# Kernel optimization log

Hardware: AMD Instinct MI355X
Metric: run time of the kernel (lower is better)

The kernel has to match this reference:

```python
import jax, jax.numpy as jnp
import numpy as np

# config constants (from init_kwargs)
DT = 1.0
TAU_J = 10.0
TAU_M = 20.0
KAPPA_J = 0.25
A_GEN = 1.0
A_DISC = 1.0
THRESH = 0.4
X_DECAY = 20.0  # trace decay constant: x += -x/20 + spikes

B = 8192
LS = [1024, 512, 512, 256]


def setup_inputs() -> dict:
    key = jax.random.key(0)
    ks = jax.random.split(key, 24)
    inp = {}
    inp['x_input'] = (jax.random.uniform(ks[0], (B, LS[0])) < 0.2).astype(jnp.float32)
    inp['y_target'] = (jax.random.uniform(ks[1], (B, LS[3])) < 0.2).astype(jnp.float32)
    # hidden-layer states (layers 1 and 2); layer 0 / last are clamped
    inp['j1'] = jax.random.normal(ks[2], (B, LS[1])) * 0.1
    inp['v1'] = jax.random.normal(ks[3], (B, LS[1])) * 0.1
    inp['s1'] = (jax.random.uniform(ks[4], (B, LS[1])) < 0.2).astype(jnp.float32)
    inp['x1'] = jax.random.uniform(ks[5], (B, LS[1])) * 2.0
    inp['j2'] = jax.random.normal(ks[6], (B, LS[2])) * 0.1
    inp['v2'] = jax.random.normal(ks[7], (B, LS[2])) * 0.1
    inp['s2'] = (jax.random.uniform(ks[8], (B, LS[2])) < 0.2).astype(jnp.float32)
    inp['x2'] = jax.random.uniform(ks[9], (B, LS[2])) * 2.0
    # weights (torch.rand * 0.01)
    inp['W0'] = jax.random.uniform(ks[10], (LS[0], LS[1])) * 0.01
    inp['W1'] = jax.random.uniform(ks[11], (LS[1], LS[2])) * 0.01
    inp['W2'] = jax.random.uniform(ks[12], (LS[2], LS[3])) * 0.01
    inp['V0'] = jax.random.uniform(ks[13], (LS[1], LS[0])) * 0.01
    inp['V1'] = jax.random.uniform(ks[14], (LS[2], LS[1])) * 0.01
    inp['V2'] = jax.random.uniform(ks[15], (LS[3], LS[2])) * 0.01
    inp['Eg0'] = jax.random.uniform(ks[16], (LS[1], LS[0])) * 0.01
    inp['Eg1'] = jax.random.uniform(ks[17], (LS[2], LS[1])) * 0.01
    inp['Eg2'] = jax.random.uniform(ks[18], (LS[3], LS[2])) * 0.01
    inp['Ed0'] = jax.random.uniform(ks[19], (LS[0], LS[1])) * 0.01
    inp['Ed1'] = jax.random.uniform(ks[20], (LS[1], LS[2])) * 0.01
    inp['Ed2'] = jax.random.uniform(ks[21], (LS[2], LS[3])) * 0.01
    return inp


def _lif_update(j, v, x, total_input):
    # Eq 19-24: leaky current integrator -> leaky membrane -> threshold -> reset -> trace
    j = j + (DT / TAU_J) * (-KAPPA_J * j + total_input)
    v = v + (DT / TAU_M) * (-v + j)  # uses updated j, as in the torch code
    spikes = (v > THRESH).astype(v.dtype)
    v = v * (1.0 - spikes)  # hard reset
    x = x + (-x / X_DECAY + spikes)  # spike trace
    return j, v, spikes, x


def reference(x_input, y_target, j1, v1, s1, x1, j2, v2, s2, x2,
              W0, W1, W2, V0, V1, V2, Eg0, Eg1, Eg2, Ed0, Ed1, Ed2):
    # --- phase 1: error neurons (all layers, using current spikes) ---
    # layer 0 clamped: x0 = x_input, s0 = x_input; layer 3 clamped: x3 = s3 = y_target
    e_gen0 = A_GEN * (x_input - s1 @ W0.T)       # [B, 1024]
    e_gen1 = A_GEN * (x1 - s2 @ W1.T)            # [B, 512]
    e_gen2 = A_GEN * (x2 - y_target @ W2.T)      # [B, 512]
    e_disc1 = A_DISC * (x1 - x_input @ V0.T)     # [B, 512]
    e_disc2 = A_DISC * (x2 - s1 @ V1.T)          # [B, 512]
    e_disc3 = A_DISC * (y_target - s2 @ V2.T)    # [B, 256]

    # --- phase 2: value-neuron updates (hidden layers 1 and 2 only) ---
    total1 = -(e_gen1 + e_disc1) + e_gen0 @ Eg0.T + e_disc2 @ Ed1.T
    total2 = -(e_gen2 + e_disc2) + e_gen1 @ Eg1.T + e_disc3 @ Ed2.T

    j1n, v1n, s1n, x1n = _lif_update(j1, v1, x1, total1)
    j2n, v2n, s2n, x2n = _lif_update(j2, v2, x2, total2)

    return jnp.concatenate([j1n, v1n, x1n, s1n, j2n, v2n, x2n, s2n], axis=-1)  # [B, 4096]
```

## Files before the change

### kernel.cpp

```cpp
#include <hip/hip_runtime.h>
#include <stdint.h>
#include <stddef.h>

typedef unsigned short u16;
typedef __attribute__((ext_vector_type(8))) short short8;
typedef __attribute__((ext_vector_type(4))) float f32x4;

#define DEVI __device__ __forceinline__

DEVI u16 f2bf(float f) {
  union { float f; unsigned u; } c; c.f = f;
  unsigned r = c.u + 0x7fff + ((c.u >> 16) & 1);
  return (u16)(r >> 16);
}

DEVI short8 pack8(f32x4 a, f32x4 b) {
  short8 v;
#pragma unroll
  for (int i = 0; i < 4; i++) { v[i] = (short)f2bf(a[i]); v[i + 4] = (short)f2bf(b[i]); }
  return v;
}

typedef __attribute__((address_space(1))) const void global_cvoid;
typedef __attribute__((address_space(3))) void lds_void;


DEVI void mfma_phase(const u16* As, const u16* Bs, f32x4 acc[4][4])
{
  const int lane = threadIdx.x & 63;
  const int w    = threadIdx.x >> 6;
  const int l16  = lane & 15, lq = lane >> 4;
  const int wm   = (w >> 1) * 64, wn = (w & 1) * 64;
#pragma unroll
  for (int kc = 0; kc < 2; kc++) {
    short8 afr[4], bfr[4];
#pragma unroll
    for (int rt = 0; rt < 4; rt++) {
      int m  = wm + rt * 16 + l16;
      int gr = (kc * 4 + lq) ^ (m & 7);
      afr[rt] = *(const short8*)(As + m * 64 + gr * 8);
    }
#pragma unroll
    for (int ct = 0; ct < 4; ct++) {
      int n  = wn + ct * 16 + l16;
      int gr = (kc * 4 + lq) ^ (n & 7);
      bfr[ct] = *(const short8*)(Bs + n * 64 + gr * 8);
    }
#pragma unroll
    for (int rt = 0; rt < 4; rt++)
#pragma unroll
      for (int ct = 0; ct < 4; ct++)
        acc[rt][ct] = __builtin_amdgcn_mfma_f32_16x16x32_bf16(afr[rt], bfr[ct], acc[rt][ct], 0, 0, 0);
  }
}

DEVI void mfma_phase32(const u16* As, const u16* Bs, f32x4 acc[2][2])
{
  const int lane = threadIdx.x & 63;
  const int w    = threadIdx.x >> 6;
  const int l16  = lane & 15, lq = lane >> 4;
  const int wm   = (w >> 1) * 32, wn = (w & 1) * 32;
#pragma unroll
  for (int kc = 0; kc < 2; kc++) {
    short8 afr[2], bfr[2];
#pragma unroll
    for (int rt = 0; rt < 2; rt++) {
      int m  = wm + rt * 16 + l16;
      int gr = (kc * 4 + lq) ^ (m & 7);
      afr[rt] = *(const short8*)(As + m * 64 + gr * 8);
    }
#pragma unroll
    for (int ct = 0; ct < 2; ct++) {
      int n  = wn + ct * 16 + l16;
      int gr = (kc * 4 + lq) ^ (n & 7);
      bfr[ct] = *(const short8*)(Bs + n * 64 + gr * 8);
    }
#pragma unroll
    for (int rt = 0; rt < 2; rt++)
#pragma unroll
      for (int ct = 0; ct < 2; ct++)
        acc[rt][ct] = __builtin_amdgcn_mfma_f32_16x16x32_bf16(afr[rt], bfr[ct], acc[rt][ct], 0, 0, 0);
  }
}

DEVI void mfma_phase64(const u16* As, const u16* Bs, f32x4 acc[2][4])
{
  const int lane = threadIdx.x & 63;
  const int w    = threadIdx.x >> 6;
  const int l16  = lane & 15, lq = lane >> 4;
  const int wm   = (w >> 1) * 32, wn = (w & 1) * 64;
#pragma unroll
  for (int kc = 0; kc < 2; kc++) {
    short8 afr[2], bfr[4];
#pragma unroll
    for (int rt = 0; rt < 2; rt++) {
      int m  = wm + rt * 16 + l16;
      int gr = (kc * 4 + lq) ^ (m & 7);
      afr[rt] = *(const short8*)(As + m * 64 + gr * 8);
    }
#pragma unroll
    for (int ct = 0; ct < 4; ct++) {
      int n  = wn + ct * 16 + l16;
      int gr = (kc * 4 + lq) ^ (n & 7);
      bfr[ct] = *(const short8*)(Bs + n * 64 + gr * 8);
    }
#pragma unroll
    for (int rt = 0; rt < 2; rt++)
#pragma unroll
      for (int ct = 0; ct < 4; ct++)
        acc[rt][ct] = __builtin_amdgcn_mfma_f32_16x16x32_bf16(afr[rt], bfr[ct], acc[rt][ct], 0, 0, 0);
  }
}

DEVI void zero_acc(f32x4 acc[4][4]) {
  f32x4 z = {0.f, 0.f, 0.f, 0.f};
#pragma unroll
  for (int a = 0; a < 4; a++)
#pragma unroll
    for (int b = 0; b < 4; b++) acc[a][b] = z;
}

DEVI void zero_acc22(f32x4 acc[2][2]) {
  f32x4 z = {0.f, 0.f, 0.f, 0.f};
#pragma unroll
  for (int a = 0; a < 2; a++)
#pragma unroll
    for (int b = 0; b < 2; b++) acc[a][b] = z;
}

DEVI void zero_acc24(f32x4 acc[2][4]) {
  f32x4 z = {0.f, 0.f, 0.f, 0.f};
#pragma unroll
  for (int a = 0; a < 2; a++)
#pragma unroll
    for (int b = 0; b < 4; b++) acc[a][b] = z;
}

struct Params {
  const float *x_input, *y_target, *j1, *v1, *s1, *x1, *j2, *v2, *s2, *x2;
  const float *W0, *W1, *W2, *V0, *V1, *V2, *Eg0, *Eg1, *Ed1, *Ed2;
};


template <int RR>
DEVI void stage_async(const u16* gbase, int ldr, int k0, u16* lds)
{
  const int t = threadIdx.x;
  const int lane = t & 63, w = t >> 6;
#pragma unroll
  for (int tt = 0; tt < RR; tt++) {
    int rowbase = w * (RR * 8) + tt * 8;
    int row = rowbase + (lane >> 3);
    int gsw = (lane & 7) ^ (row & 7);
    __builtin_amdgcn_global_load_lds(
        (global_cvoid*)(gbase + (size_t)row * ldr + k0 + gsw * 8),
        (lds_void*)(lds + rowbase * 64), 16, 0, 0);
  }
}

DEVI void gemm_term64(const u16* A, const u16* B, int K,
                      u16* As, u16* Bs, f32x4 acc[2][2])
{
  for (int k0 = 0; k0 < K; k0 += 64) {
    stage_async<2>(A, K, k0, As);
    stage_async<2>(B, K, k0, Bs);
    __syncthreads();
    mfma_phase32(As, Bs, acc);
    __syncthreads();
  }
}

DEVI void gemm_term_pp(const u16* A, const u16* B, int K,
                       u16* As0, u16* As1, u16* Bs0, u16* Bs1, f32x4 acc[2][4])
{
  const int nk = K >> 6;
  stage_async<2>(A, K, 0, As0);
  stage_async<4>(B, K, 0, Bs0);
  __syncthreads();
  for (int t = 0; t < nk; t++) {
    if (t + 1 < nk) {
      if (t & 1) { stage_async<2>(A, K, (t + 1) * 64, As0); stage_async<4>(B, K, (t + 1) * 64, Bs0); }
      else       { stage_async<2>(A, K, (t + 1) * 64, As1); stage_async<4>(B, K, (t + 1) * 64, Bs1); }
    }
    if (t & 1) mfma_phase64(As1, Bs1, acc);
    else       mfma_phase64(As0, Bs0, acc);
    __syncthreads();
  }
}

struct PJob { const float *s0, *s1; u16* dst; int start; };
struct TJob { const float* in; u16* out; int J, tbase; };
struct PrepArgs { PJob jb[14]; TJob tj[4]; };

__global__ __launch_bounds__(256) void k_prep(PrepArgs A)
{
  __shared__ u16 T[32][33];
  int b = blockIdx.x;
  int t = threadIdx.x;
  if (b < 14464) {
    int ji = 0;
#pragma unroll
    for (int i = 1; i < 14; i++)
      if (b >= A.jb[i].start) ji = i;
    PJob pj = A.jb[ji];
    size_t e0 = ((size_t)(b - pj.start) * 256 + t) * 8;
    const float* s0 = pj.s0 + e0;
    f32x4 a  = *(const f32x4*)s0;
    f32x4 b4 = *(const f32x4*)(s0 + 4);
    if (pj.s1) {
      const float* s1 = pj.s1 + e0;
      a  = a  + *(const f32x4*)s1;
      b4 = b4 + *(const f32x4*)(s1 + 4);
    }
    *(short8*)(pj.dst + e0) = pack8(a, b4);
    return;
  }
  int b2 = b - 14464;
  int ji = 0;
#pragma unroll
  for (int i = 1; i < 4; i++)
    if (b2 >= A.tj[i].tbase) ji = i;
  TJob jb = A.tj[ji];
  int local = b2 - jb.tbase;
  int tm = local >> 4;
  int tk = local & 15;
  int tx = t & 31, ty = t >> 5;
#pragma unroll
  for (int i = 0; i < 4; i++) {
    int r = ty + i * 8;
    T[r][tx] = f2bf(jb.in[(size_t)(tm * 32 + r) * 512 + tk * 32 + tx]);
  }
  __syncthreads();
#pragma unroll
  for (int i = 0; i < 4; i++) {
    int r = ty + i * 8;
    jb.out[(size_t)(tk * 32 + r) * jb.J + tm * 32 + tx] = T[tx][r];
  }
}

struct BW2Args {
  const u16 *Eg0b, *W0tb, *Ed1b, *V1tb, *Eg1b, *W1tb, *Ed2b, *V2tb;
  u16 *Bw1b, *Bw2b;
};

__global__ __launch_bounds__(256) void k_bw2(BW2Args A)
{
  __shared__ u16 As[64 * 64];
  __shared__ u16 Bs[64 * 64];
  int b   = blockIdx.x;
  int mat = b >> 6, loc = b & 63;
  int bmw = loc >> 3, bnw = loc & 7;

  f32x4 acc[2][2];
  zero_acc22(acc);
  u16* dst;
  if (mat == 0) {
    gemm_term64(A.Eg0b + (size_t)bmw * 64 * 1024, A.W0tb + (size_t)bnw * 64 * 1024, 1024, As, Bs, acc);
    gemm_term64(A.Ed1b + (size_t)bmw * 64 * 512,  A.V1tb + (size_t)bnw * 64 * 512,   512, As, Bs, acc);
    dst = A.Bw1b;
  } else {
    gemm_term64(A.Eg1b + (size_t)bmw * 64 * 512,  A.W1tb + (size_t)bnw * 64 * 512,   512, As, Bs, acc);
    gemm_term64(A.Ed2b + (size_t)bmw * 64 * 256,  A.V2tb + (size_t)bnw * 64 * 256,   256, As, Bs, acc);
    dst = A.Bw2b;
  }
  const int lane = threadIdx.x & 63;
  const int w    = threadIdx.x >> 6;
  const int l16  = lane & 15, lq = lane >> 4;
  const int wm   = (w >> 1) * 32, wn = (w & 1) * 32;
#pragma unroll
  for (int rt = 0; rt < 2; rt++)
#pragma unroll
    for (int ct = 0; ct < 2; ct++)
#pragma unroll
      for (int i = 0; i < 4; i++) {
        int rl = wm + rt * 16 + lq * 4 + i;
        int cl = wn + ct * 16 + l16;
        dst[(size_t)(bmw * 64 + rl) * 512 + bnw * 64 + cl] = f2bf(-acc[rt][ct][i]);
      }
}

struct MJobF {
  const u16* A[4]; const u16* B[4]; int K[4];
  const float *jin, *vin, *xin;
  int obase;
};
struct MArgsF { MJobF j[2]; };

__global__ __launch_bounds__(256, 3) void k_main_fast(MArgsF P, float* __restrict__ out)
{
  __shared__ u16 As0[64 * 64];
  __shared__ u16 As1[64 * 64];
  __shared__ u16 Bs0[128 * 64];
  __shared__ u16 Bs1[128 * 64];
  int bid   = blockIdx.x;
  int job   = bid >> 9;
  int local = bid & 511;
  int bm = local & 127, bn = local >> 7;
  MJobF jb = P.j[job];

  switch (((bid >> 8) ^ bid) & 3) {
    case 1: __builtin_amdgcn_s_sleep(8); break;
    case 2: __builtin_amdgcn_s_sleep(8); __builtin_amdgcn_s_sleep(8); break;
    case 3: __builtin_amdgcn_s_sleep(8); __builtin_amdgcn_s_sleep(8);
            __builtin_amdgcn_s_sleep(8); break;
    default: break;
  }

  f32x4 acc[2][4];
  zero_acc24(acc);
#pragma unroll
  for (int p = 0; p < 4; p++)
    gemm_term_pp(jb.A[p] + (size_t)bm * 64 * jb.K[p],
                 jb.B[p] + (size_t)bn * 128 * jb.K[p], jb.K[p],
                 As0, As1, Bs0, Bs1, acc);

  const int lane = threadIdx.x & 63;
  const int w    = threadIdx.x >> 6;
  const int l16  = lane & 15, lq = lane >> 4;
  const int wm   = (w >> 1) * 32, wn = (w & 1) * 64;

#pragma unroll
  for (int rt = 0; rt < 2; rt++)
#pragma unroll
    for (int ct = 0; ct < 4; ct++)
#pragma unroll
      for (int i = 0; i < 4; i++) {
        int row    = bm * 64 + wm + rt * 16 + lq * 4 + i;
        int col    = bn * 128 + wn + ct * 16 + l16;
        size_t idx = (size_t)row * 512 + col;
        float xf = jb.xin[idx];
        float total = acc[rt][ct][i] - 2.0f * xf;
        float jf = jb.jin[idx];
        float vf = jb.vin[idx];
        jf = jf + 0.1f * (-0.25f * jf + total);
        vf = vf + 0.05f * (-vf + jf);
        float sf = (vf > 0.4f) ? 1.0f : 0.0f;
        vf = vf * (1.0f - sf);
        xf = xf + (-xf / 20.0f + sf);
        size_t ob = (size_t)row * 4096 + jb.obase + col;
        out[ob]        = jf;
        out[ob + 512]  = vf;
        out[ob + 1024] = xf;
        out[ob + 1536] = sf;
      }
}


DEVI void stage_A_fb(const float* A, int ldr, int k0, u16* dst)
{
  const int t = threadIdx.x;
  const int g = t & 7, rb = t >> 3;
#pragma unroll
  for (int p = 0; p < 4; p++) {
    int row = p * 32 + rb;
    const float* src = A + (size_t)row * ldr + k0 + g * 8;
    f32x4 a = *(const f32x4*)src;
    f32x4 b = *(const f32x4*)(src + 4);
    *(short8*)(dst + row * 64 + (g ^ (row & 7)) * 8) = pack8(a, b);
  }
}

DEVI void nn_term_fb(const float* A, const float* B, int K, u16* As, u16* Bs, f32x4 acc[4][4])
{
  const int t  = threadIdx.x;
  const int ks = t >> 4, ng = t & 15;
  for (int k0 = 0; k0 < K; k0 += 64) {
    stage_A_fb(A, K, k0, As);
#pragma unroll
    for (int i = 0; i < 4; i++) {
      int kloc = i * 16 + ks;
      const float* src = B + (size_t)(k0 + kloc) * 512 + ng * 8;
      f32x4 a = *(const f32x4*)src;
      f32x4 b = *(const f32x4*)(src + 4);
#pragma unroll
      for (int e = 0; e < 8; e++) {
        int nloc = ng * 8 + e;
        float val = (e < 4) ? a[e] : b[e - 4];
        Bs[nloc * 64 + ((kloc >> 3) ^ (nloc & 7)) * 8 + (kloc & 7)] = f2bf(val);
      }
    }
    __syncthreads();
    mfma_phase(As, Bs, acc);
    __syncthreads();
  }
}

template <int MODE>
DEVI void gemm_term_fb(const float* A, const float* B0, const float* B1, int K,
                       u16* As, u16* Bs, f32x4 acc[4][4])
{
  const int t = threadIdx.x;
  const int g = t & 7, rb = t >> 3;
  for (int k0 = 0; k0 < K; k0 += 64) {
    stage_A_fb(A, K, k0, As);
#pragma unroll
    for (int p = 0; p < 4; p++) {
      int row = p * 32 + rb;
      const float* src;
      if (MODE == 2) src = B0 + (size_t)row * 4096 + (k0 >> 7) * 512 + (k0 & 127) + g * 8;
      else           src = B0 + (size_t)row * K + k0 + g * 8;
      f32x4 a = *(const f32x4*)src;
      f32x4 b = *(const f32x4*)(src + 4);
      if (MODE == 1) {
        const float* s2 = B1 + (size_t)row * K + k0 + g * 8;
        a = a + *(const f32x4*)s2;
        b = b + *(const f32x4*)(s2 + 4);
      }
      *(short8*)(Bs + row * 64 + (g ^ (row & 7)) * 8) = pack8(a, b);
    }
    __syncthreads();
    mfma_phase(As, Bs, acc);
    __syncthreads();
  }
}

__global__ __launch_bounds__(256) void k_bw_fb(Params P, float* __restrict__ out)
{
  __shared__ u16 As[128 * 64];
  __shared__ u16 Bs[128 * 64];
  int b   = blockIdx.x;
  int mat = b >> 4, loc = b & 15;
  int bmw = loc >> 2, bnw = loc & 3;

  f32x4 acc[4][4];
  zero_acc(acc);
  int obase;
  if (mat == 0) {
    nn_term_fb(P.Eg0 + (size_t)bmw * 128 * 1024, P.W0 + bnw * 128, 1024, As, Bs, acc);
    nn_term_fb(P.Ed1 + (size_t)bmw * 128 * 512,  P.V1 + bnw * 128,  512, As, Bs, acc);
    obase = 0;
  } else {
    nn_term_fb(P.Eg1 + (size_t)bmw * 128 * 512,  P.W1 + bnw * 128,  512, As, Bs, acc);
    nn_term_fb(P.Ed2 + (size_t)bmw * 128 * 256,  P.V2 + bnw * 128,  256, As, Bs, acc);
    obase = 2048;
  }
  const int lane = threadIdx.x & 63;
  const int w    = threadIdx.x >> 6;
  const int l16  = lane & 15, lq = lane >> 4;
  const int wm   = (w >> 1) * 64, wn = (w & 1) * 64;
#pragma unroll
  for (int rt = 0; rt < 4; rt++)
#pragma unroll
    for (int ct = 0; ct < 4; ct++)
#pragma unroll
      for (int i = 0; i < 4; i++) {
        int rl = wm + rt * 16 + lq * 4 + i;
        int cl = wn + ct * 16 + l16;
        out[(size_t)rl * 4096 + obase + bmw * 128 + bnw * 512 + cl] = -acc[rt][ct][i];
      }
}

__global__ __launch_bounds__(256) void k_main_fb(Params P, float* __restrict__ out, int fix)
{
  __shared__ u16 As[128 * 64];
  __shared__ u16 Bs[128 * 64];
  int job, bm, bn;
  if (fix) {
    job = blockIdx.x >> 2; bn = blockIdx.x & 3; bm = 0;
  } else {
    job = blockIdx.x >> 8;
    int local = blockIdx.x & 255;
    bm = local & 63; bn = local >> 6;
    if (bm == 0) return;
  }

  f32x4 acc[4][4];
  zero_acc(acc);
  const float *jin, *vin, *xin;
  int obase;
  size_t am = (size_t)bm * 128;

  if (job == 0) {
    gemm_term_fb<0>(P.s2      + am * 512,  P.W1  + (size_t)bn * 128 * 512,  nullptr, 512,  As, Bs, acc);
    gemm_term_fb<1>(P.x_input + am * 1024, P.V0  + (size_t)bn * 128 * 1024,
                    P.Eg0 + (size_t)bn * 128 * 1024, 1024, As, Bs, acc);
    gemm_term_fb<0>(P.x2      + am * 512,  P.Ed1 + (size_t)bn * 128 * 512,  nullptr, 512,  As, Bs, acc);
    gemm_term_fb<2>(P.s1      + am * 512,  out + 0 + bn * 128,              nullptr, 512,  As, Bs, acc);
    jin = P.j1; vin = P.v1; xin = P.x1; obase = 0;
  } else {
    gemm_term_fb<1>(P.y_target + am * 256, P.W2  + (size_t)bn * 128 * 256,
                    P.Ed2 + (size_t)bn * 128 * 256, 256, As, Bs, acc);
    gemm_term_fb<0>(P.s1      + am * 512,  P.V1  + (size_t)bn * 128 * 512,  nullptr, 512,  As, Bs, acc);
    gemm_term_fb<0>(P.x1      + am * 512,  P.Eg1 + (size_t)bn * 128 * 512,  nullptr, 512,  As, Bs, acc);
    gemm_term_fb<2>(P.s2      + am * 512,  out + 2048 + bn * 128,           nullptr, 512,  As, Bs, acc);
    jin = P.j2; vin = P.v2; xin = P.x2; obase = 2048;
  }

  const int lane = threadIdx.x & 63;
  const int w    = threadIdx.x >> 6;
  const int l16  = lane & 15, lq = lane >> 4;
  const int wm   = (w >> 1) * 64, wn = (w & 1) * 64;

#pragma unroll
  for (int rt = 0; rt < 4; rt++)
#pragma unroll
    for (int ct = 0; ct < 4; ct++)
#pragma unroll
      for (int i = 0; i < 4; i++) {
        int row    = bm * 128 + wm + rt * 16 + lq * 4 + i;
        int col    = bn * 128 + wn + ct * 16 + l16;
        size_t idx = (size_t)row * 512 + col;
        float xf = xin[idx];
        float total = acc[rt][ct][i] - 2.0f * xf;
        float jf = jin[idx];
        float vf = vin[idx];
        jf = jf + 0.1f * (-0.25f * jf + total);
        vf = vf + 0.05f * (-vf + jf);
        float sf = (vf > 0.4f) ? 1.0f : 0.0f;
        vf = vf * (1.0f - sf);
        xf = xf + (-xf / 20.0f + sf);
        size_t ob = (size_t)row * 4096 + obase + col;
        out[ob]        = jf;
        out[ob + 512]  = vf;
        out[ob + 1024] = xf;
        out[ob + 1536] = sf;
      }
}

extern "C" void kernel_launch(void* const* d_in, const int* in_sizes, int n_in,
                              void* d_out, int out_size, void* d_ws, size_t ws_size,
                              hipStream_t stream)
{
  Params P;
  P.x_input  = (const float*)d_in[0];
  P.y_target = (const float*)d_in[1];
  P.j1 = (const float*)d_in[2];
  P.v1 = (const float*)d_in[3];
  P.s1 = (const float*)d_in[4];
  P.x1 = (const float*)d_in[5];
  P.j2 = (const float*)d_in[6];
  P.v2 = (const float*)d_in[7];
  P.s2 = (const float*)d_in[8];
  P.x2 = (const float*)d_in[9];
  P.W0 = (const float*)d_in[10];
  P.W1 = (const float*)d_in[11];
  P.W2 = (const float*)d_in[12];
  P.V0 = (const float*)d_in[13];
  P.V1 = (const float*)d_in[14];
  P.V2 = (const float*)d_in[15];
  P.Eg0 = (const float*)d_in[16];
  P.Eg1 = (const float*)d_in[17];
  P.Ed1 = (const float*)d_in[20];
  P.Ed2 = (const float*)d_in[21];
  (void)in_sizes; (void)n_in; (void)out_size;

  float* out = (float*)d_out;

  if (ws_size >= 62652416) {
    char* ws = (char*)d_ws;
    u16* xin_b = (u16*)(ws + 0);
    u16* y_b   = (u16*)(ws + 16777216);
    u16* s1_b  = (u16*)(ws + 20971520);
    u16* x1_b  = (u16*)(ws + 29360128);
    u16* s2_b  = (u16*)(ws + 37748736);
    u16* x2_b  = (u16*)(ws + 46137344);
    u16* W1_b  = (u16*)(ws + 54525952);
    u16* P1_b  = (u16*)(ws + 55050240);
    u16* Ed1_b = (u16*)(ws + 56098816);
    u16* V1_b  = (u16*)(ws + 56623104);
    u16* Eg1_b = (u16*)(ws + 57147392);
    u16* P2_b  = (u16*)(ws + 57671680);
    u16* Bw1_b = (u16*)(ws + 57933824);
    u16* Bw2_b = (u16*)(ws + 58458112);
    u16* W0t_b = (u16*)(ws + 58982400);
    u16* V1t_b = (u16*)(ws + 60030976);
    u16* W1t_b = (u16*)(ws + 60555264);
    u16* V2t_b = (u16*)(ws + 61079552);
    u16* Eg0_b = (u16*)(ws + 61341696);
    u16* Ed2_b = (u16*)(ws + 62390272);

    PrepArgs pa;
    pa.jb[0]  = { P.x_input,  nullptr, xin_b,     0 };
    pa.jb[1]  = { P.y_target, nullptr, y_b,    4096 };
    pa.jb[2]  = { P.s1,       nullptr, s1_b,   5120 };
    pa.jb[3]  = { P.x1,       nullptr, x1_b,   7168 };
    pa.jb[4]  = { P.s2,       nullptr, s2_b,   9216 };
    pa.jb[5]  = { P.x2,       nullptr, x2_b,  11264 };
    pa.jb[6]  = { P.W1,       nullptr, W1_b,  13312 };
    pa.jb[7]  = { P.V0,       P.Eg0,   P1_b,  13440 };
    pa.jb[8]  = { P.Ed1,      nullptr, Ed1_b, 13696 };
    pa.jb[9]  = { P.V1,       nullptr, V1_b,  13824 };
    pa.jb[10] = { P.Eg1,      nullptr, Eg1_b, 13952 };
    pa.jb[11] = { P.W2,       P.Ed2,   P2_b,  14080 };
    pa.jb[12] = { P.Eg0,      nullptr, Eg0_b, 14144 };
    pa.jb[13] = { P.Ed2,      nullptr, Ed2_b, 14400 };
    pa.tj[0]  = { P.W0, W0t_b, 1024,    0 };
    pa.tj[1]  = { P.V1, V1t_b,  512,  512 };
    pa.tj[2]  = { P.W1, W1t_b,  512,  768 };
    pa.tj[3]  = { P.V2, V2t_b,  256, 1024 };
    k_prep<<<dim3(15616), dim3(256), 0, stream>>>(pa);

    BW2Args ba;
    ba.Eg0b = Eg0_b; ba.W0tb = W0t_b; ba.Ed1b = Ed1_b; ba.V1tb = V1t_b;
    ba.Eg1b = Eg1_b; ba.W1tb = W1t_b; ba.Ed2b = Ed2_b; ba.V2tb = V2t_b;
    ba.Bw1b = Bw1_b; ba.Bw2b = Bw2_b;
    k_bw2<<<dim3(128), dim3(256), 0, stream>>>(ba);

    MArgsF ma;
    ma.j[0].A[0] = s2_b;  ma.j[0].B[0] = W1_b;  ma.j[0].K[0] = 512;
    ma.j[0].A[1] = xin_b; ma.j[0].B[1] = P1_b;  ma.j[0].K[1] = 1024;
    ma.j[0].A[2] = x2_b;  ma.j[0].B[2] = Ed1_b; ma.j[0].K[2] = 512;
    ma.j[0].A[3] = s1_b;  ma.j[0].B[3] = Bw1_b; ma.j[0].K[3] = 512;
    ma.j[0].jin = P.j1; ma.j[0].vin = P.v1; ma.j[0].xin = P.x1; ma.j[0].obase = 0;
    ma.j[1].A[0] = y_b;   ma.j[1].B[0] = P2_b;  ma.j[1].K[0] = 256;
    ma.j[1].A[1] = s1_b;  ma.j[1].B[1] = V1_b;  ma.j[1].K[1] = 512;
    ma.j[1].A[2] = x1_b;  ma.j[1].B[2] = Eg1_b; ma.j[1].K[2] = 512;
    ma.j[1].A[3] = s2_b;  ma.j[1].B[3] = Bw2_b; ma.j[1].K[3] = 512;
    ma.j[1].jin = P.j2; ma.j[1].vin = P.v2; ma.j[1].xin = P.x2; ma.j[1].obase = 2048;
    k_main_fast<<<dim3(1024), dim3(256), 0, stream>>>(ma, out);
  } else {
    k_bw_fb<<<dim3(32), dim3(256), 0, stream>>>(P, out);
    k_main_fb<<<dim3(512), dim3(256), 0, stream>>>(P, out, 0);
    k_main_fb<<<dim3(8), dim3(256), 0, stream>>>(P, out, 1);
  }
}
```

Baseline: 419.0 us.

## Overlap weight-product GEMM with activation conversion; single-buffer main GEMM for occupancy

The prep kernel is split so that only the inputs the small weight-product GEMM needs (the transposes plus Eg0, Ed2, Ed1, Eg1) are converted first. The bulk activation fp32-to-bf16 conversion now runs in the same launch as that GEMM, with 4 chunks per block, so the 128 GEMM blocks overlap with conversion work instead of running alone on a mostly idle device. Separately, the main fused GEMM drops LDS double-buffering for a single buffer and raises the launch-bounds occupancy hint from 3 to 4 blocks. This trades prefetch overlap for more resident blocks and could lose latency hiding in the main kernel.

Result: faster. 387.6 us (-7.5%).

```diff
diff --git a/kernel.cpp b/kernel.cpp
--- a/kernel.cpp
+++ b/kernel.cpp
@@ -170,58 +170,56 @@
   }
 }
 
-DEVI void gemm_term_pp(const u16* A, const u16* B, int K,
-                       u16* As0, u16* As1, u16* Bs0, u16* Bs1, f32x4 acc[2][4])
-{
-  const int nk = K >> 6;
-  stage_async<2>(A, K, 0, As0);
-  stage_async<4>(B, K, 0, Bs0);
-  __syncthreads();
-  for (int t = 0; t < nk; t++) {
-    if (t + 1 < nk) {
-      if (t & 1) { stage_async<2>(A, K, (t + 1) * 64, As0); stage_async<4>(B, K, (t + 1) * 64, Bs0); }
-      else       { stage_async<2>(A, K, (t + 1) * 64, As1); stage_async<4>(B, K, (t + 1) * 64, Bs1); }
-    }
-    if (t & 1) mfma_phase64(As1, Bs1, acc);
-    else       mfma_phase64(As0, Bs0, acc);
+DEVI void gemm_term_main(const u16* A, const u16* B, int K,
+                         u16* As, u16* Bs, f32x4 acc[2][4])
+{
+  for (int k0 = 0; k0 < K; k0 += 64) {
+    stage_async<2>(A, K, k0, As);
+    stage_async<4>(B, K, k0, Bs);
+    __syncthreads();
+    mfma_phase64(As, Bs, acc);
     __syncthreads();
   }
 }
 
 struct PJob { const float *s0, *s1; u16* dst; int start; };
+
+DEVI void do_convert_chunk(const PJob& pj, int c, int t)
+{
+  size_t e0 = ((size_t)(c - pj.start) * 256 + t) * 8;
+  const float* s0 = pj.s0 + e0;
+  f32x4 a  = *(const f32x4*)s0;
+  f32x4 b4 = *(const f32x4*)(s0 + 4);
+  if (pj.s1) {
+    const float* s1 = pj.s1 + e0;
+    a  = a  + *(const f32x4*)s1;
+    b4 = b4 + *(const f32x4*)(s1 + 4);
+  }
+  *(short8*)(pj.dst + e0) = pack8(a, b4);
+}
+
 struct TJob { const float* in; u16* out; int J, tbase; };
-struct PrepArgs { PJob jb[14]; TJob tj[4]; };
-
-__global__ __launch_bounds__(256) void k_prep(PrepArgs A)
+struct PrepAArgs { TJob tj[4]; PJob jb[4]; };
+
+__global__ __launch_bounds__(256) void k_prep_a(PrepAArgs A)
 {
   __shared__ u16 T[32][33];
   int b = blockIdx.x;
   int t = threadIdx.x;
-  if (b < 14464) {
+  if (b >= 1152) {
     int ji = 0;
 #pragma unroll
-    for (int i = 1; i < 14; i++)
+    for (int i = 1; i < 4; i++)
       if (b >= A.jb[i].start) ji = i;
-    PJob pj = A.jb[ji];
-    size_t e0 = ((size_t)(b - pj.start) * 256 + t) * 8;
-    const float* s0 = pj.s0 + e0;
-    f32x4 a  = *(const f32x4*)s0;
-    f32x4 b4 = *(const f32x4*)(s0 + 4);
-    if (pj.s1) {
-      const float* s1 = pj.s1 + e0;
-      a  = a  + *(const f32x4*)s1;
-      b4 = b4 + *(const f32x4*)(s1 + 4);
-    }
-    *(short8*)(pj.dst + e0) = pack8(a, b4);
+    do_convert_chunk(A.jb[ji], b, t);
     return;
   }
-  int b2 = b - 14464;
   int ji = 0;
 #pragma unroll
   for (int i = 1; i < 4; i++)
-    if (b2 >= A.tj[i].tbase) ji = i;
+    if (b >= A.tj[i].tbase) ji = i;
   TJob jb = A.tj[ji];
-  int local = b2 - jb.tbase;
+  int local = b - jb.tbase;
   int tm = local >> 4;
   int tk = local & 15;
   int tx = t & 31, ty = t >> 5;
@@ -238,45 +236,60 @@
   }
 }
 
-struct BW2Args {
+struct MergedArgs {
   const u16 *Eg0b, *W0tb, *Ed1b, *V1tb, *Eg1b, *W1tb, *Ed2b, *V2tb;
   u16 *Bw1b, *Bw2b;
+  PJob jb[10];
 };
 
-__global__ __launch_bounds__(256) void k_bw2(BW2Args A)
+__global__ __launch_bounds__(256) void k_merged(MergedArgs A)
 {
   __shared__ u16 As[64 * 64];
   __shared__ u16 Bs[64 * 64];
-  int b   = blockIdx.x;
-  int mat = b >> 6, loc = b & 63;
-  int bmw = loc >> 3, bnw = loc & 7;
-
-  f32x4 acc[2][2];
-  zero_acc22(acc);
-  u16* dst;
-  if (mat == 0) {
-    gemm_term64(A.Eg0b + (size_t)bmw * 64 * 1024, A.W0tb + (size_t)bnw * 64 * 1024, 1024, As, Bs, acc);
-    gemm_term64(A.Ed1b + (size_t)bmw * 64 * 512,  A.V1tb + (size_t)bnw * 64 * 512,   512, As, Bs, acc);
-    dst = A.Bw1b;
-  } else {
-    gemm_term64(A.Eg1b + (size_t)bmw * 64 * 512,  A.W1tb + (size_t)bnw * 64 * 512,   512, As, Bs, acc);
-    gemm_term64(A.Ed2b + (size_t)bmw * 64 * 256,  A.V2tb + (size_t)bnw * 64 * 256,   256, As, Bs, acc);
-    dst = A.Bw2b;
-  }
-  const int lane = threadIdx.x & 63;
-  const int w    = threadIdx.x >> 6;
-  const int l16  = lane & 15, lq = lane >> 4;
-  const int wm   = (w >> 1) * 32, wn = (w & 1) * 32;
-#pragma unroll
-  for (int rt = 0; rt < 2; rt++)
-#pragma unroll
-    for (int ct = 0; ct < 2; ct++)
-#pragma unroll
-      for (int i = 0; i < 4; i++) {
-        int rl = wm + rt * 16 + lq * 4 + i;
-        int cl = wn + ct * 16 + l16;
-        dst[(size_t)(bmw * 64 + rl) * 512 + bnw * 64 + cl] = f2bf(-acc[rt][ct][i]);
-      }
+  int b = blockIdx.x;
+  int t = threadIdx.x;
+
+  if (b < 128) {
+    int mat = b >> 6, loc = b & 63;
+    int bmw = loc >> 3, bnw = loc & 7;
+    f32x4 acc[2][2];
+    zero_acc22(acc);
+    u16* dst;
+    if (mat == 0) {
+      gemm_term64(A.Eg0b + (size_t)bmw * 64 * 1024, A.W0tb + (size_t)bnw * 64 * 1024, 1024, As, Bs, acc);
+      gemm_term64(A.Ed1b + (size_t)bmw * 64 * 512,  A.V1tb + (size_t)bnw * 64 * 512,   512, As, Bs, acc);
+      dst = A.Bw1b;
+    } else {
+      gemm_term64(A.Eg1b + (size_t)bmw * 64 * 512,  A.W1tb + (size_t)bnw * 64 * 512,   512, As, Bs, acc);
+      gemm_term64(A.Ed2b + (size_t)bmw * 64 * 256,  A.V2tb + (size_t)bnw * 64 * 256,   256, As, Bs, acc);
+      dst = A.Bw2b;
+    }
+    const int lane = t & 63;
+    const int w    = t >> 6;
+    const int l16  = lane & 15, lq = lane >> 4;
+    const int wm   = (w >> 1) * 32, wn = (w & 1) * 32;
+#pragma unroll
+    for (int rt = 0; rt < 2; rt++)
+#pragma unroll
+      for (int ct = 0; ct < 2; ct++)
+#pragma unroll
+        for (int i = 0; i < 4; i++) {
+          int rl = wm + rt * 16 + lq * 4 + i;
+          int cl = wn + ct * 16 + l16;
+          dst[(size_t)(bmw * 64 + rl) * 512 + bnw * 64 + cl] = f2bf(-acc[rt][ct][i]);
+        }
+    return;
+  }
+
+  int cb = (b - 128) * 4;
+  for (int it = 0; it < 4; it++) {
+    int c = cb + it;
+    int ji = 0;
+#pragma unroll
+    for (int i = 1; i < 10; i++)
+      if (c >= A.jb[i].start) ji = i;
+    do_convert_chunk(A.jb[ji], c, t);
+  }
 }
 
 struct MJobF {
@@ -286,12 +299,10 @@
 };
 struct MArgsF { MJobF j[2]; };
 
-__global__ __launch_bounds__(256, 3) void k_main_fast(MArgsF P, float* __restrict__ out)
-{
-  __shared__ u16 As0[64 * 64];
-  __shared__ u16 As1[64 * 64];
-  __shared__ u16 Bs0[128 * 64];
-  __shared__ u16 Bs1[128 * 64];
+__global__ __launch_bounds__(256, 4) void k_main_fast(MArgsF P, float* __restrict__ out)
+{
+  __shared__ u16 As[64 * 64];
+  __shared__ u16 Bs[128 * 64];
   int bid   = blockIdx.x;
   int job   = bid >> 9;
   int local = bid & 511;
@@ -310,9 +321,8 @@
   zero_acc24(acc);
 #pragma unroll
   for (int p = 0; p < 4; p++)
-    gemm_term_pp(jb.A[p] + (size_t)bm * 64 * jb.K[p],
-                 jb.B[p] + (size_t)bn * 128 * jb.K[p], jb.K[p],
-                 As0, As1, Bs0, Bs1, acc);
+    gemm_term_main(jb.A[p] + (size_t)bm * 64 * jb.K[p],
+                   jb.B[p] + (size_t)bn * 128 * jb.K[p], jb.K[p], As, Bs, acc);
 
   const int lane = threadIdx.x & 63;
   const int w    = threadIdx.x >> 6;
@@ -569,32 +579,32 @@
     u16* Eg0_b = (u16*)(ws + 61341696);
     u16* Ed2_b = (u16*)(ws + 62390272);
 
-    PrepArgs pa;
-    pa.jb[0]  = { P.x_input,  nullptr, xin_b,     0 };
-    pa.jb[1]  = { P.y_target, nullptr, y_b,    4096 };
-    pa.jb[2]  = { P.s1,       nullptr, s1_b,   5120 };
-    pa.jb[3]  = { P.x1,       nullptr, x1_b,   7168 };
-    pa.jb[4]  = { P.s2,       nullptr, s2_b,   9216 };
-    pa.jb[5]  = { P.x2,       nullptr, x2_b,  11264 };
-    pa.jb[6]  = { P.W1,       nullptr, W1_b,  13312 };
-    pa.jb[7]  = { P.V0,       P.Eg0,   P1_b,  13440 };
-    pa.jb[8]  = { P.Ed1,      nullptr, Ed1_b, 13696 };
-    pa.jb[9]  = { P.V1,       nullptr, V1_b,  13824 };
-    pa.jb[10] = { P.Eg1,      nullptr, Eg1_b, 13952 };
-    pa.jb[11] = { P.W2,       P.Ed2,   P2_b,  14080 };
-    pa.jb[12] = { P.Eg0,      nullptr, Eg0_b, 14144 };
-    pa.jb[13] = { P.Ed2,      nullptr, Ed2_b, 14400 };
-    pa.tj[0]  = { P.W0, W0t_b, 1024,    0 };
-    pa.tj[1]  = { P.V1, V1t_b,  512,  512 };
-    pa.tj[2]  = { P.W1, W1t_b,  512,  768 };
-    pa.tj[3]  = { P.V2, V2t_b,  256, 1024 };
-    k_prep<<<dim3(15616), dim3(256), 0, stream>>>(pa);
-
-    BW2Args ba;
-    ba.Eg0b = Eg0_b; ba.W0tb = W0t_b; ba.Ed1b = Ed1_b; ba.V1tb = V1t_b;
-    ba.Eg1b = Eg1_b; ba.W1tb = W1t_b; ba.Ed2b = Ed2_b; ba.V2tb = V2t_b;
-    ba.Bw1b = Bw1_b; ba.Bw2b = Bw2_b;
-    k_bw2<<<dim3(128), dim3(256), 0, stream>>>(ba);
+    PrepAArgs paa;
+    paa.tj[0] = { P.W0, W0t_b, 1024,    0 };
+    paa.tj[1] = { P.V1, V1t_b,  512,  512 };
+    paa.tj[2] = { P.W1, W1t_b,  512,  768 };
+    paa.tj[3] = { P.V2, V2t_b,  256, 1024 };
+    paa.jb[0] = { P.Eg0, nullptr, Eg0_b, 1152 };
+    paa.jb[1] = { P.Ed2, nullptr, Ed2_b, 1408 };
+    paa.jb[2] = { P.Ed1, nullptr, Ed1_b, 1472 };
+    paa.jb[3] = { P.Eg1, nullptr, Eg1_b, 1600 };
+    k_prep_a<<<dim3(1728), dim3(256), 0, stream>>>(paa);
+
+    MergedArgs mg;
+    mg.Eg0b = Eg0_b; mg.W0tb = W0t_b; mg.Ed1b = Ed1_b; mg.V1tb = V1t_b;
+    mg.Eg1b = Eg1_b; mg.W1tb = W1t_b; mg.Ed2b = Ed2_b; mg.V2tb = V2t_b;
+    mg.Bw1b = Bw1_b; mg.Bw2b = Bw2_b;
+    mg.jb[0] = { P.x_input,  nullptr, xin_b,     0 };
+    mg.jb[1] = { P.y_target, nullptr, y_b,    4096 };
+    mg.jb[2] = { P.s1,       nullptr, s1_b,   5120 };
+    mg.jb[3] = { P.x1,       nullptr, x1_b,   7168 };
+    mg.jb[4] = { P.s2,       nullptr, s2_b,   9216 };
+    mg.jb[5] = { P.x2,       nullptr, x2_b,  11264 };
+    mg.jb[6] = { P.W1,       nullptr, W1_b,  13312 };
+    mg.jb[7] = { P.V0,       P.Eg0,   P1_b,  13440 };
+    mg.jb[8] = { P.V1,       nullptr, V1_b,  13696 };
+    mg.jb[9] = { P.W2,       P.Ed2,   P2_b,  13824 };
+    k_merged<<<dim3(3600), dim3(256), 0, stream>>>(mg);
 
     MArgsF ma;
     ma.j[0].A[0] = s2_b;  ma.j[0].B[0] = W1_b;  ma.j[0].K[0] = 512;
```
